# Optimization experiments

Measured on AMD Instinct MI355X. Metric: run time of the kernel, lower is better.

The kernel has to match this reference:

```python
import jax, jax.numpy as jnp
import numpy as np

HIDDEN = 2048
N_HEADS = 32
N_KV_HEADS = 8
HEAD_DIM = 64
ROPE_THETA = 500000.0
B, S = 1, 2048


def _rope_tables(seq_len):
    inv_freq = 1.0 / ROPE_THETA ** (jnp.arange(0, HEAD_DIM, 2, dtype=jnp.float32) / HEAD_DIM)
    angles = jnp.arange(seq_len, dtype=jnp.float32)[:, None] * inv_freq[None, :]
    return jnp.cos(angles), jnp.sin(angles)


def _apply_rope(x, cos, sin):
    # x: (B, S, H, D); cos/sin: (S, D//2)
    x1 = x[..., 0::2]
    x2 = x[..., 1::2]
    c = cos[None, :, None, :]
    s = sin[None, :, None, :]
    x1r = x1 * c - x2 * s
    x2r = x1 * s + x2 * c
    return jnp.stack([x1r, x2r], axis=-1).reshape(x.shape)


def setup_inputs() -> dict:
    key = jax.random.key(0)
    ks = jax.random.split(key, 5)
    hidden_states = jax.random.normal(ks[0], (B, S, HIDDEN), dtype=jnp.float32)
    # causal mask, broadcastable over (B, H, S, S)
    attention_mask = jnp.tril(jnp.ones((S, S), dtype=bool))[None, :, :]
    sc = 1.0 / np.sqrt(HIDDEN)
    wq = jax.random.normal(ks[1], (HIDDEN, N_HEADS * HEAD_DIM), dtype=jnp.float32) * sc
    wk = jax.random.normal(ks[2], (HIDDEN, N_KV_HEADS * HEAD_DIM), dtype=jnp.float32) * sc
    wv = jax.random.normal(ks[3], (HIDDEN, N_KV_HEADS * HEAD_DIM), dtype=jnp.float32) * sc
    wo = jax.random.normal(ks[4], (N_HEADS * HEAD_DIM, HIDDEN), dtype=jnp.float32) * sc
    return {"hidden_states": hidden_states, "attention_mask": attention_mask,
            "wq": wq, "wk": wk, "wv": wv, "wo": wo}


def reference(hidden_states, attention_mask, wq, wk, wv, wo):
    b, s, _ = hidden_states.shape
    groups = N_HEADS // N_KV_HEADS
    q = (hidden_states @ wq).reshape(b, s, N_HEADS, HEAD_DIM)
    k = (hidden_states @ wk).reshape(b, s, N_KV_HEADS, HEAD_DIM)
    v = (hidden_states @ wv).reshape(b, s, N_KV_HEADS, HEAD_DIM)
    cos, sin = _rope_tables(s)
    q = _apply_rope(q, cos, sin)
    k = _apply_rope(k, cos, sin)
    k = jnp.repeat(k, groups, axis=2)  # (b, s, H, D)
    v = jnp.repeat(v, groups, axis=2)
    q = q.transpose(0, 2, 1, 3)  # (b, H, s, D)
    k = k.transpose(0, 2, 1, 3)
    v = v.transpose(0, 2, 1, 3)
    scores = jnp.einsum('bhqd,bhkd->bhqk', q, k) / jnp.sqrt(jnp.float32(HEAD_DIM))
    scores = jnp.where(attention_mask[:, None, :, :], scores, -jnp.inf)
    probs = jax.nn.softmax(scores, axis=-1)
    out = jnp.einsum('bhqk,bhkd->bhqd', probs, v)
    out = out.transpose(0, 2, 1, 3).reshape(b, s, N_HEADS * HEAD_DIM)
    return out @ wo
```

## Files before the change

### kernel.cpp

```cpp
#include <hip/hip_runtime.h>

typedef __attribute__((ext_vector_type(8))) short short8;
typedef __attribute__((ext_vector_type(4))) float float4v;

union U4S8 { uint4 u; short8 s; };

__device__ __forceinline__ float bf2f(ushort u) {
    union { uint i; float f; } v; v.i = ((uint)u) << 16; return v.f;
}
__device__ __forceinline__ ushort f2bf(float f) {
    union { uint i; float f; } v; v.f = f;
    return (ushort)((v.i + 0x7FFFu + ((v.i >> 16) & 1u)) >> 16);
}
#if __has_builtin(__builtin_amdgcn_cvt_pk_bf16_f32)
__device__ __forceinline__ uint f2bf_pk(float a, float b) {
    auto r = __builtin_amdgcn_cvt_pk_bf16_f32(a, b);
    return __builtin_bit_cast(uint, r);
}
#else
__device__ __forceinline__ uint f2bf_pk(float a, float b) {
    return (uint)f2bf(a) | ((uint)f2bf(b) << 16);
}
#endif
__device__ __forceinline__ void gld_lds16(const ushort* g, ushort* l) {
    __builtin_amdgcn_global_load_lds((const __attribute__((address_space(1))) unsigned int*)g,
                                     (__attribute__((address_space(3))) unsigned int*)l,
                                     16, 0, 0);
}

__device__ __forceinline__ void tconv_body(const float* in, ushort* out,
                                           int C, int r0, int c0, int tid) {
    __shared__ float t[64][65];
    const int lrow = tid >> 2;
    const int lc   = (tid & 3) * 16;
    const float* ip = in + (size_t)(r0 + lrow) * C + c0 + lc;
#pragma unroll
    for (int i = 0; i < 4; i++) {
        float4 v = *(const float4*)(ip + 4 * i);
        t[lrow][lc + 4 * i + 0] = v.x; t[lrow][lc + 4 * i + 1] = v.y;
        t[lrow][lc + 4 * i + 2] = v.z; t[lrow][lc + 4 * i + 3] = v.w;
    }
    __syncthreads();
    ushort* op = out + (size_t)(c0 + lrow) * 2048 + r0 + lc;
#pragma unroll
    for (int i = 0; i < 8; i++)
        ((uint*)op)[i] = f2bf_pk(t[lc + 2 * i][lrow], t[lc + 2 * i + 1][lrow]);
}

__global__ __launch_bounds__(256) void prep(const float* __restrict__ hidden,
                                            const float* __restrict__ wq,
                                            const float* __restrict__ wk,
                                            const float* __restrict__ wv,
                                            const float* __restrict__ wo,
                                            ushort* __restrict__ hid,
                                            ushort* __restrict__ wT,
                                            ushort* __restrict__ woT) {
    const int bx = blockIdx.x;
    if (bx < 2048) {
        const size_t i = ((size_t)bx * 256 + threadIdx.x) * 8;
        float4 a = *(const float4*)(hidden + i);
        float4 b = *(const float4*)(hidden + i + 4);
        uint4 u;
        u.x = f2bf_pk(a.x, a.y); u.y = f2bf_pk(a.z, a.w);
        u.z = f2bf_pk(b.x, b.y); u.w = f2bf_pk(b.z, b.w);
        *(uint4*)(hid + i) = u;
    } else if (bx < 3584) {
        const int i = bx - 2048;
        const int xx = i % 48, yy = i / 48;
        const float* in; ushort* op; int C, cx;
        if (xx < 32)      { in = wq; op = wT;                        C = 2048; cx = xx; }
        else if (xx < 40) { in = wk; op = wT + (size_t)2048 * 2048;  C = 512;  cx = xx - 32; }
        else              { in = wv; op = wT + (size_t)2560 * 2048;  C = 512;  cx = xx - 40; }
        tconv_body(in, op, C, yy * 64, cx * 64, threadIdx.x);
    } else {
        const int i = bx - 3584;
        tconv_body(wo, woT, 2048, (i >> 5) * 64, (i & 31) * 64, threadIdx.x);
    }
}

template <int NBF, bool BF16OUT, bool ROPE>
__global__ __launch_bounds__(512, 2) void gemm_k2048(const ushort* __restrict__ A,
                                                     const ushort* __restrict__ Bt,
                                                     void* __restrict__ Cout,
                                                     int N, int lda) {
    constexpr int BN  = 32 * NBF;
    constexpr int BCH = BN / 16;
    __shared__ ushort As[4][128 * 32];
    __shared__ ushort Bs[4][BN * 32];

    const int tid = threadIdx.x, w = tid >> 6, lane = tid & 63;
    const int lr = lane & 15, quad = lane >> 4;
    const int m0 = blockIdx.x * 128, n0 = blockIdx.y * BN;
    const int wr = w >> 1, wc = w & 1;

    const int srow = lane >> 2;
    const int skb  = (lane & 3) ^ ((srow >> 1) & 3);

    const ushort* ApW  = A  + (size_t)(m0 + 16 * w + srow) * lda + skb * 8;
    const ushort* BpW  = Bt + (size_t)(n0 + 16 * w + srow) * 2048 + skb * 8;
    const ushort* BpW2 = Bt + (size_t)(n0 + 128 + 16 * w + srow) * 2048 + skb * 8;

    float4v acc[2][NBF];
#pragma unroll
    for (int a = 0; a < 2; a++)
#pragma unroll
        for (int b = 0; b < NBF; b++) { acc[a][b][0] = 0.f; acc[a][b][1] = 0.f; acc[a][b][2] = 0.f; acc[a][b][3] = 0.f; }

    const int fsw = (lr >> 1) & 3;

#pragma unroll
    for (int p = 0; p < 3; p++) {
        gld_lds16(ApW + 32 * p, &As[p][w * 512]);
        gld_lds16(BpW + 32 * p, &Bs[p][w * 512]);
        if constexpr (BCH > 8)
            if (w < BCH - 8) gld_lds16(BpW2 + 32 * p, &Bs[p][(8 + w) * 512]);
    }

#define GSTEP(IT, BUF, PBUF, WAITSTR, PF)                                                 \
    {                                                                                     \
        asm volatile("s_waitcnt " WAITSTR " lgkmcnt(0)\n\ts_barrier" ::: "memory");       \
        if (PF) {                                                                         \
            const int kp_ = ((IT) + 3) << 5;                                              \
            gld_lds16(ApW + kp_, &As[PBUF][w * 512]);                                     \
            gld_lds16(BpW + kp_, &Bs[PBUF][w * 512]);                                     \
            if constexpr (BCH > 8)                                                        \
                if (w < BCH - 8) gld_lds16(BpW2 + kp_, &Bs[PBUF][(8 + w) * 512]);         \
        }                                                                                 \
        short8 af[2], bf[NBF];                                                            \
        _Pragma("unroll")                                                                 \
        for (int mt = 0; mt < 2; mt++)                                                    \
            af[mt] = *(const short8*)&As[BUF][(wr * 32 + mt * 16 + lr) * 32 + (quad ^ fsw) * 8]; \
        _Pragma("unroll")                                                                 \
        for (int nt = 0; nt < NBF; nt++)                                                  \
            bf[nt] = *(const short8*)&Bs[BUF][(wc * 16 * NBF + nt * 16 + lr) * 32 + (quad ^ fsw) * 8]; \
        _Pragma("unroll")                                                                 \
        for (int mt = 0; mt < 2; mt++)                                                    \
            _Pragma("unroll")                                                             \
            for (int nt = 0; nt < NBF; nt++)                                              \
                acc[mt][nt] = __builtin_amdgcn_mfma_f32_16x16x32_bf16(af[mt], bf[nt], acc[mt][nt], 0, 0, 0); \
    }

    for (int it = 0; it < 60; it += 4) {
        GSTEP(it + 0, 0, 3, "vmcnt(4)", true);
        GSTEP(it + 1, 1, 0, "vmcnt(4)", true);
        GSTEP(it + 2, 2, 1, "vmcnt(4)", true);
        GSTEP(it + 3, 3, 2, "vmcnt(4)", true);
    }
    GSTEP(60, 0, 3, "vmcnt(4)", true);
    GSTEP(61, 1, 0, "vmcnt(4)", false);
    GSTEP(62, 2, 1, "vmcnt(2)", false);
    GSTEP(63, 3, 2, "vmcnt(0)", false);
#undef GSTEP

    const int rbase = m0 + wr * 32 + quad * 4;
    const int cbase = n0 + wc * 16 * NBF + lr;
    if (BF16OUT) {
        ushort* Cb = (ushort*)Cout;
#pragma unroll
        for (int nt = 0; nt < NBF; nt++) {
            const int col = cbase + nt * 16;
            if (ROPE && col < 2560) {
                const float osc = (col < 2048) ? 0.18033688f : 1.0f;
                const float sgn = (lr & 1) ? 1.0f : -1.0f;
                const int j = (col >> 1) & 31;
                const float inv = __expf(-(float)(2 * j) * (1.0f / 64.0f) * 13.122363377404328f);
#pragma unroll
                for (int mt = 0; mt < 2; mt++)
#pragma unroll
                    for (int r = 0; r < 4; r++) {
                        const int row = rbase + mt * 16 + r;
                        float sn, cs;
                        sincosf((float)row * inv, &sn, &cs);
                        const float mine = acc[mt][nt][r];
                        const float partner = __shfl_xor(mine, 1);
                        Cb[(size_t)row * N + col] = f2bf((mine * cs + sgn * partner * sn) * osc);
                    }
            } else {
#pragma unroll
                for (int mt = 0; mt < 2; mt++)
#pragma unroll
                    for (int r = 0; r < 4; r++)
                        Cb[(size_t)(rbase + mt * 16 + r) * N + col] = f2bf(acc[mt][nt][r]);
            }
        }
    } else {
        float* Cf = (float*)Cout;
#pragma unroll
        for (int mt = 0; mt < 2; mt++)
#pragma unroll
            for (int nt = 0; nt < NBF; nt++)
#pragma unroll
                for (int r = 0; r < 4; r++)
                    Cf[(size_t)(rbase + mt * 16 + r) * N + cbase + nt * 16] = acc[mt][nt][r];
    }
}

__global__ __launch_bounds__(256) void attn_mfma(const ushort* __restrict__ Q,
                                                 const ushort* __restrict__ Kc,
                                                 const ushort* __restrict__ Vc,
                                                 ushort* __restrict__ O0,
                                                 ushort* __restrict__ O1,
                                                 float* __restrict__ L0,
                                                 float* __restrict__ L1) {
    __shared__ ushort Ks[2][64 * 64];
    __shared__ ushort Vt[2][64 * 64];
    __shared__ ushort Ps[4][16 * 64];

    const int tid = threadIdx.x, w = tid >> 6, lane = tid & 63;
    const int lr = lane & 15, quad = lane >> 4;
    const int h = blockIdx.y, g = h >> 2, z = blockIdx.z;

    const int dg = tid & 15;
    const int kl = tid >> 4;
    const int ksub = lane >> 3, dsub = lane & 7;
    ushort* Pw = Ps[w];
    ushort* Op = z ? O1 : O0;
    float*  Lp = z ? L1 : L0;

    const ushort* Vp0 = Vc + g * 64 + dg * 4 + (size_t)3072 * kl;
    const ushort* Kp0 = Kc + g * 64 + ((dsub ^ ksub) * 8) + (size_t)3072 * ksub;

    short8 onesf;
#pragma unroll
    for (int j = 0; j < 8; j++) onesf[j] = (short)0x3F80;

    for (int ti = 0; ti < 2; ti++) {
        const int bx = ti ? 31 - (int)blockIdx.x : (int)blockIdx.x;
        const int nch = (bx >= z) ? ((bx - z) >> 1) + 1 : 0;
        const int last = z + 2 * (nch - 1);

        const ushort* qp = Q + (size_t)(bx * 64 + w * 16 + lr) * 3072 + h * 64 + quad * 8;
        const short8 qf0 = *(const short8*)qp;
        const short8 qf1 = *(const short8*)(qp + 32);

        float4v oacc[4], lacc;
#pragma unroll
        for (int t = 0; t < 4; t++) { oacc[t][0] = 0.f; oacc[t][1] = 0.f; oacc[t][2] = 0.f; oacc[t][3] = 0.f; }
        lacc[0] = 0.f; lacc[1] = 0.f; lacc[2] = 0.f; lacc[3] = 0.f;

        uint2 vv[4];
        if (nch) {
#pragma unroll
            for (int t = 0; t < 4; t++)
                vv[t] = *(const uint2*)(Vp0 + (size_t)(z * 64 + 16 * t) * 3072);
        }
        __syncthreads();
        if (nch) {
#pragma unroll
            for (int i = 0; i < 2; i++) {
                const int rt = 2 * w + i;
                gld_lds16(Kp0 + (size_t)(z * 64 + rt * 8) * 3072, &Ks[0][rt * 512]);
            }
        }

        for (int c = 0; c < nch; c++) {
            const int kb = z + 2 * c;
            const int b = c & 1;
            ushort* bKs = Ks[b];
            ushort* bVt = Vt[b];

#pragma unroll
            for (int i = 0; i < 4; i++) {
                const uint sel = (i & 1) ? 0x07060302u : 0x05040100u;
                uint s0 = (i < 2) ? vv[0].x : vv[0].y;
                uint s1 = (i < 2) ? vv[1].x : vv[1].y;
                uint s2 = (i < 2) ? vv[2].x : vv[2].y;
                uint s3 = (i < 2) ? vv[3].x : vv[3].y;
                uint2 pk;
                pk.x = __builtin_amdgcn_perm(s1, s0, sel);
                pk.y = __builtin_amdgcn_perm(s3, s2, sel);
                *(uint2*)&bVt[(dg * 4 + i) * 64 + (kl ^ ((dg & 3) * 4 + i)) * 4] = pk;
            }

            const int kn = (c + 1 < nch) ? kb + 2 : last;
#pragma unroll
            for (int t = 0; t < 4; t++)
                vv[t] = *(const uint2*)(Vp0 + (size_t)(kn * 64 + 16 * t) * 3072);

            asm volatile("s_waitcnt vmcnt(4) lgkmcnt(0)\n\ts_barrier" ::: "memory");

#pragma unroll
            for (int i = 0; i < 2; i++) {
                const int rt = 2 * w + i;
                gld_lds16(Kp0 + (size_t)(kn * 64 + rt * 8) * 3072, &Ks[1 - b][rt * 512]);
            }

            float4v sacc[4];
#pragma unroll
            for (int t = 0; t < 4; t++) { sacc[t][0] = 0.f; sacc[t][1] = 0.f; sacc[t][2] = 0.f; sacc[t][3] = 0.f; }
#pragma unroll
            for (int t = 0; t < 4; t++) {
                const int krow = t * 16 + lr;
                const int sw = lr & 7;
                short8 kf0 = *(const short8*)&bKs[krow * 64 + ((quad)     ^ sw) * 8];
                short8 kf1 = *(const short8*)&bKs[krow * 64 + ((quad + 4) ^ sw) * 8];
                sacc[t] = __builtin_amdgcn_mfma_f32_16x16x32_bf16(qf0, kf0, sacc[t], 0, 0, 0);
                sacc[t] = __builtin_amdgcn_mfma_f32_16x16x32_bf16(qf1, kf1, sacc[t], 0, 0, 0);
            }

            if (kb == bx) {
#pragma unroll
                for (int r = 0; r < 4; r++) {
                    const int qr = w * 16 + quad * 4 + r;
                    float p0 = exp2f(sacc[0][r]), p1 = exp2f(sacc[1][r]);
                    float p2 = exp2f(sacc[2][r]), p3 = exp2f(sacc[3][r]);
                    if (lr > qr)      p0 = 0.f;
                    if (16 + lr > qr) p1 = 0.f;
                    if (32 + lr > qr) p2 = 0.f;
                    if (48 + lr > qr) p3 = 0.f;
                    const int prow = quad * 4 + r;
                    uint2 pk; pk.x = f2bf_pk(p0, p1); pk.y = f2bf_pk(p2, p3);
                    *(uint2*)&Pw[prow * 64 + (lr ^ prow) * 4] = pk;
                }
            } else {
#pragma unroll
                for (int r = 0; r < 4; r++) {
                    const int prow = quad * 4 + r;
                    uint2 pk;
                    pk.x = f2bf_pk(exp2f(sacc[0][r]), exp2f(sacc[1][r]));
                    pk.y = f2bf_pk(exp2f(sacc[2][r]), exp2f(sacc[3][r]));
                    *(uint2*)&Pw[prow * 64 + (lr ^ prow) * 4] = pk;
                }
            }

#pragma unroll
            for (int ks2 = 0; ks2 < 2; ks2++) {
                const int ub = ks2 * 8 + quad * 2;
                U4S8 pu;
                uint2 plo = *(const uint2*)&Pw[lr * 64 + ((ub)     ^ lr) * 4];
                uint2 phi = *(const uint2*)&Pw[lr * 64 + ((ub + 1) ^ lr) * 4];
                pu.u.x = plo.x; pu.u.y = plo.y; pu.u.z = phi.x; pu.u.w = phi.y;
                lacc = __builtin_amdgcn_mfma_f32_16x16x32_bf16(pu.s, onesf, lacc, 0, 0, 0);
#pragma unroll
                for (int t = 0; t < 4; t++) {
                    const int d = t * 16 + lr;
                    U4S8 vu;
                    uint2 vlo = *(const uint2*)&bVt[d * 64 + ((ub)     ^ lr) * 4];
                    uint2 vhi = *(const uint2*)&bVt[d * 64 + ((ub + 1) ^ lr) * 4];
                    vu.u.x = vlo.x; vu.u.y = vlo.y; vu.u.z = vhi.x; vu.u.w = vhi.y;
                    oacc[t] = __builtin_amdgcn_mfma_f32_16x16x32_bf16(pu.s, vu.s, oacc[t], 0, 0, 0);
                }
            }
        }

        ushort* op = Op + (size_t)(bx * 64 + w * 16 + quad * 4) * 2048 + h * 64 + lr;
#pragma unroll
        for (int t = 0; t < 4; t++)
#pragma unroll
            for (int r = 0; r < 4; r++)
                op[(size_t)r * 2048 + t * 16] = f2bf(oacc[t][r]);
        if (lr == 0) {
#pragma unroll
            for (int r = 0; r < 4; r++)
                Lp[h * 2048 + bx * 64 + w * 16 + quad * 4 + r] = lacc[r];
        }
    }
}

__global__ __launch_bounds__(256) void combine(ushort* __restrict__ O0,
                                               const ushort* __restrict__ O1,
                                               const float* __restrict__ L0,
                                               const float* __restrict__ L1) {
    const int idx = blockIdx.x * 256 + threadIdx.x;
    const int r = idx >> 8;
    const int c8 = (idx & 255) * 8;
    const int h = c8 >> 6;
    const float rl = 1.0f / (L0[h * 2048 + r] + L1[h * 2048 + r]);
    uint4 a = *(const uint4*)(O0 + (size_t)r * 2048 + c8);
    uint4 b = *(const uint4*)(O1 + (size_t)r * 2048 + c8);
    uint ua[4] = {a.x, a.y, a.z, a.w}, ub[4] = {b.x, b.y, b.z, b.w};
    uint rr[4];
#pragma unroll
    for (int k = 0; k < 4; k++) {
        float x0 = bf2f((ushort)(ua[k] & 0xFFFFu)) + bf2f((ushort)(ub[k] & 0xFFFFu));
        float x1 = bf2f((ushort)(ua[k] >> 16))     + bf2f((ushort)(ub[k] >> 16));
        rr[k] = f2bf_pk(x0 * rl, x1 * rl);
    }
    uint4 res; res.x = rr[0]; res.y = rr[1]; res.z = rr[2]; res.w = rr[3];
    *(uint4*)(O0 + (size_t)r * 2048 + c8) = res;
}

extern "C" void kernel_launch(void* const* d_in, const int* in_sizes, int n_in,
                              void* d_out, int out_size, void* d_ws, size_t ws_size,
                              hipStream_t stream) {
    const float* hidden = (const float*)d_in[0];
    const float* wq = (const float*)d_in[2];
    const float* wk = (const float*)d_in[3];
    const float* wv = (const float*)d_in[4];
    const float* wo = (const float*)d_in[5];

    ushort* ws = (ushort*)d_ws;
    ushort* hid = ws;
    ushort* wT  = ws + 4194304;
    ushort* woT = ws + 10485760;
    ushort* O1  = wT;
    float*  L0  = (float*)(ws + 8388608);
    float*  L1  = L0 + 65536;
    ushort* QKV = (ushort*)d_out;

    prep<<<4608, 256, 0, stream>>>(hidden, wq, wk, wv, wo, hid, wT, woT);
    gemm_k2048<6, true, true><<<dim3(16, 16), 512, 0, stream>>>(hid, wT, QKV, 3072, 2048);
    attn_mfma<<<dim3(16, 32, 2), 256, 0, stream>>>(QKV, QKV + 2048, QKV + 2560,
                                                   hid , O1, L0, L1);
    combine<<<2048, 256, 0, stream>>>(hid, O1, L0, L1);
    gemm_k2048<4, false, false><<<dim3(16, 16), 512, 0, stream>>>(hid, woT, d_out, 2048, 2048);
}
```

Before: 238.3 us.

## Load GEMM A operand directly from global into registers, bypassing LDS

The K=2048 GEMM no longer stages the A tile through shared memory. Each wave now loads its A fragments from global memory straight into a 4-slot register ring two steps ahead, while B still uses async LDS staging. The vmcnt waits are adjusted per wave to match the new load counts. This cuts LDS traffic and footprint, but duplicates A global reads across the two column waves and uses more registers.

```diff
diff --git a/kernel.cpp b/kernel.cpp
--- a/kernel.cpp
+++ b/kernel.cpp
@@ -79,13 +79,12 @@
 }
 
 template <int NBF, bool BF16OUT, bool ROPE>
-__global__ __launch_bounds__(512, 2) void gemm_k2048(const ushort* __restrict__ A,
-                                                     const ushort* __restrict__ Bt,
-                                                     void* __restrict__ Cout,
-                                                     int N, int lda) {
+__global__ __launch_bounds__(512, 2) void gemm_adirect(const ushort* __restrict__ A,
+                                                       const ushort* __restrict__ Bt,
+                                                       void* __restrict__ Cout,
+                                                       int N, int lda) {
     constexpr int BN  = 32 * NBF;
     constexpr int BCH = BN / 16;
-    __shared__ ushort As[4][128 * 32];
     __shared__ ushort Bs[4][BN * 32];
 
     const int tid = threadIdx.x, w = tid >> 6, lane = tid & 63;
@@ -96,10 +95,11 @@
     const int srow = lane >> 2;
     const int skb  = (lane & 3) ^ ((srow >> 1) & 3);
 
-    const ushort* ApW  = A  + (size_t)(m0 + 16 * w + srow) * lda + skb * 8;
     const ushort* BpW  = Bt + (size_t)(n0 + 16 * w + srow) * 2048 + skb * 8;
     const ushort* BpW2 = Bt + (size_t)(n0 + 128 + 16 * w + srow) * 2048 + skb * 8;
 
+    const ushort* Aq = A + (size_t)(m0 + wr * 32 + lr) * lda + quad * 8;
+
     float4v acc[2][NBF];
 #pragma unroll
     for (int a = 0; a < 2; a++)
@@ -108,49 +108,66 @@
 
     const int fsw = (lr >> 1) & 3;
 
-#pragma unroll
-    for (int p = 0; p < 3; p++) {
-        gld_lds16(ApW + 32 * p, &As[p][w * 512]);
-        gld_lds16(BpW + 32 * p, &Bs[p][w * 512]);
-        if constexpr (BCH > 8)
-            if (w < BCH - 8) gld_lds16(BpW2 + 32 * p, &Bs[p][(8 + w) * 512]);
-    }
-
-#define GSTEP(IT, BUF, PBUF, WAITSTR, PF)                                                 \
+    short8 af[4][2];
+
+#define STAGE_B(P, BUF)                                                                   \
     {                                                                                     \
-        asm volatile("s_waitcnt " WAITSTR " lgkmcnt(0)\n\ts_barrier" ::: "memory");       \
-        if (PF) {                                                                         \
-            const int kp_ = ((IT) + 3) << 5;                                              \
-            gld_lds16(ApW + kp_, &As[PBUF][w * 512]);                                     \
-            gld_lds16(BpW + kp_, &Bs[PBUF][w * 512]);                                     \
-            if constexpr (BCH > 8)                                                        \
-                if (w < BCH - 8) gld_lds16(BpW2 + kp_, &Bs[PBUF][(8 + w) * 512]);         \
-        }                                                                                 \
-        short8 af[2], bf[NBF];                                                            \
-        _Pragma("unroll")                                                                 \
-        for (int mt = 0; mt < 2; mt++)                                                    \
-            af[mt] = *(const short8*)&As[BUF][(wr * 32 + mt * 16 + lr) * 32 + (quad ^ fsw) * 8]; \
+        gld_lds16(BpW + ((P) << 5), &Bs[BUF][w * 512]);                                   \
+        if constexpr (BCH > 8)                                                            \
+            if (w < BCH - 8) gld_lds16(BpW2 + ((P) << 5), &Bs[BUF][(8 + w) * 512]);       \
+    }
+#define LOAD_A(IT, SLOT)                                                                  \
+    {                                                                                     \
+        af[SLOT][0] = *(const short8*)(Aq + ((IT) << 5));                                 \
+        af[SLOT][1] = *(const short8*)(Aq + 16 * lda + ((IT) << 5));                      \
+    }
+
+    STAGE_B(0, 0);
+    STAGE_B(1, 1);
+    LOAD_A(0, 0);
+    STAGE_B(2, 2);
+    LOAD_A(1, 1);
+
+#define GSTEP(IT, WS, PFB, PFA)                                                           \
+    {                                                                                     \
+        asm volatile("s_waitcnt " WS " lgkmcnt(0)\n\ts_barrier" ::: "memory");            \
+        if (PFB) STAGE_B((IT) + 3, ((IT) + 3) & 3);                                       \
+        if (PFA) LOAD_A((IT) + 2, ((IT) + 2) & 3);                                        \
+        short8 bf[NBF];                                                                   \
         _Pragma("unroll")                                                                 \
         for (int nt = 0; nt < NBF; nt++)                                                  \
-            bf[nt] = *(const short8*)&Bs[BUF][(wc * 16 * NBF + nt * 16 + lr) * 32 + (quad ^ fsw) * 8]; \
+            bf[nt] = *(const short8*)&Bs[(IT) & 3][(wc * 16 * NBF + nt * 16 + lr) * 32 + (quad ^ fsw) * 8]; \
         _Pragma("unroll")                                                                 \
         for (int mt = 0; mt < 2; mt++)                                                    \
             _Pragma("unroll")                                                             \
             for (int nt = 0; nt < NBF; nt++)                                              \
-                acc[mt][nt] = __builtin_amdgcn_mfma_f32_16x16x32_bf16(af[mt], bf[nt], acc[mt][nt], 0, 0, 0); \
-    }
-
-    for (int it = 0; it < 60; it += 4) {
-        GSTEP(it + 0, 0, 3, "vmcnt(4)", true);
-        GSTEP(it + 1, 1, 0, "vmcnt(4)", true);
-        GSTEP(it + 2, 2, 1, "vmcnt(4)", true);
-        GSTEP(it + 3, 3, 2, "vmcnt(4)", true);
-    }
-    GSTEP(60, 0, 3, "vmcnt(4)", true);
-    GSTEP(61, 1, 0, "vmcnt(4)", false);
-    GSTEP(62, 2, 1, "vmcnt(2)", false);
-    GSTEP(63, 3, 2, "vmcnt(0)", false);
+                acc[mt][nt] = __builtin_amdgcn_mfma_f32_16x16x32_bf16(af[(IT) & 3][mt], bf[nt], acc[mt][nt], 0, 0, 0); \
+    }
+
+#define KLOOP(WS)                                                                         \
+    {                                                                                     \
+        for (int it = 0; it < 60; it += 4) {                                              \
+            GSTEP(it + 0, WS, 1, 1);                                                      \
+            GSTEP(it + 1, WS, 1, 1);                                                      \
+            GSTEP(it + 2, WS, 1, 1);                                                      \
+            GSTEP(it + 3, WS, 1, 1);                                                      \
+        }                                                                                 \
+        GSTEP(60, WS, 1, 1);                                                              \
+        GSTEP(61, WS, 0, 1);                                                              \
+        GSTEP(62, "vmcnt(2)", 0, 0);                                                      \
+        GSTEP(63, "vmcnt(0)", 0, 0);                                                      \
+    }
+
+    if constexpr (BCH > 8) {
+        if (w < BCH - 8) KLOOP("vmcnt(4)")
+        else             KLOOP("vmcnt(3)")
+    } else {
+        KLOOP("vmcnt(3)")
+    }
+#undef KLOOP
 #undef GSTEP
+#undef LOAD_A
+#undef STAGE_B
 
     const int rbase = m0 + wr * 32 + quad * 4;
     const int cbase = n0 + wc * 16 * NBF + lr;
@@ -399,9 +416,9 @@
     ushort* QKV = (ushort*)d_out;
 
     prep<<<4608, 256, 0, stream>>>(hidden, wq, wk, wv, wo, hid, wT, woT);
-    gemm_k2048<6, true, true><<<dim3(16, 16), 512, 0, stream>>>(hid, wT, QKV, 3072, 2048);
+    gemm_adirect<6, true, true><<<dim3(16, 16), 512, 0, stream>>>(hid, wT, QKV, 3072, 2048);
     attn_mfma<<<dim3(16, 32, 2), 256, 0, stream>>>(QKV, QKV + 2048, QKV + 2560,
                                                    hid , O1, L0, L1);
     combine<<<2048, 256, 0, stream>>>(hid, O1, L0, L1);
-    gemm_k2048<4, false, false><<<dim3(16, 16), 512, 0, stream>>>(hid, woT, d_out, 2048, 2048);
-}
+    gemm_adirect<4, false, false><<<dim3(16, 16), 512, 0, stream>>>(hid, woT, d_out, 2048, 2048);
+}
```

Measured after the change: 260.0 us. +9.1%, slower.
